# Kernel optimization log

Measured on AMD Instinct MI355X. Metric: run time of the kernel, lower is better.

## Reference

```python
import jax, jax.numpy as jnp
import numpy as np

B, C, H, W = 4, 256, 48, 48
NH = 8
HD = C // NH
SCALE = HD ** -0.5


def setup_inputs() -> dict:
    key = jax.random.key(0)
    ks = jax.random.split(key, 9)
    std = 1.0 / np.sqrt(C)
    return {
        "x": jax.random.normal(ks[0], (B, C, H, W), dtype=jnp.float32),
        "Wq": jax.random.normal(ks[1], (C, C), dtype=jnp.float32) * std,
        "bq": jax.random.normal(ks[2], (C,), dtype=jnp.float32) * std,
        "Wk": jax.random.normal(ks[3], (C, C), dtype=jnp.float32) * std,
        "bk": jax.random.normal(ks[4], (C,), dtype=jnp.float32) * std,
        "Wv": jax.random.normal(ks[5], (C, C), dtype=jnp.float32) * std,
        "bv": jax.random.normal(ks[6], (C,), dtype=jnp.float32) * std,
        "Wo": jax.random.normal(ks[7], (C, C), dtype=jnp.float32) * std,
        "bo": jax.random.normal(ks[8], (C,), dtype=jnp.float32) * std,
    }


def _proj(x, Wm, bm):
    # 1x1 conv == pointwise channel matmul; x: [B,C,H,W], Wm: [out,in]
    return jnp.einsum('bchw,oc->bohw', x, Wm) + bm[None, :, None, None]


def reference(x, Wq, bq, Wk, bk, Wv, bv, Wo, bo):
    b, c, h, w = x.shape
    s = h * w
    # [B,C,H,W] -> [B, NH, S, HD]
    def heads(t):
        return t.reshape(b, NH, HD, s).transpose(0, 1, 3, 2)
    q = heads(_proj(x, Wq, bq))
    k = heads(_proj(x, Wk, bk))
    v = heads(_proj(x, Wv, bv))
    attn = jax.nn.softmax(jnp.einsum('bhsd,bhtd->bhst', q, k) * SCALE, axis=-1)
    out = jnp.einsum('bhst,bhtd->bhsd', attn, v)
    out = out.transpose(0, 1, 3, 2).reshape(b, c, h, w)
    out = _proj(out, Wo, bo)
    return out + x
```

## Files before the change

### kernel.cpp

```cpp
#include <hip/hip_runtime.h>
#include <hip/hip_bf16.h>

#define BATCH 4
#define CCH   256
#define SS    2304
#define NHEAD 8
#define HD    32
#define SCALE_L2E (1.4426950408889634f * 0.17677669529663687f)

using bf16x8 = __attribute__((ext_vector_type(8))) short;
using v4s    = __attribute__((ext_vector_type(4))) short;
using v8s    = __attribute__((ext_vector_type(8))) short;
using f32x4  = __attribute__((ext_vector_type(4))) float;

static __device__ __forceinline__ unsigned short f2bf(float f) {
    union { float f; unsigned u; } a; a.f = f;
    unsigned r = a.u + 0x7fff + ((a.u >> 16) & 1);
    return (unsigned short)(r >> 16);
}
static __device__ __forceinline__ unsigned pk2(float a, float b) {
    return (unsigned)f2bf(a) | ((unsigned)f2bf(b) << 16);
}
static __device__ __forceinline__ v4s pack4(float a, float b, float c, float d) {
    float2 lo; lo.x = a; lo.y = b;
    float2 hi; hi.x = c; hi.y = d;
    union { __hip_bfloat162 h2[2]; v4s s; } u;
    u.h2[0] = __float22bfloat162_rn(lo);
    u.h2[1] = __float22bfloat162_rn(hi);
    return u.s;
}

__global__ __launch_bounds__(256) void wconv(const float* __restrict__ Wq, const float* __restrict__ Wk,
                                             const float* __restrict__ Wv, const float* __restrict__ Wo,
                                             unsigned short* __restrict__ wqkv, unsigned short* __restrict__ wo) {
    const int idx = blockIdx.x * 256 + threadIdx.x;
    if (idx < 768 * 256) {
        const int o = idx >> 8, c = idx & 255;
        const float v = (o < 256) ? Wq[idx] : (o < 512) ? Wk[(o - 256) * 256 + c] : Wv[(o - 512) * 256 + c];
        wqkv[idx] = f2bf(v);
    } else {
        const int j = idx - 768 * 256;
        wo[j] = f2bf(Wo[j]);
    }
}

__global__ __launch_bounds__(256) void xtrans(const float* __restrict__ x, unsigned short* __restrict__ xt) {
    __shared__ float T[64][65];
    const int b = blockIdx.z, c0 = blockIdx.y * 64, s0 = blockIdx.x * 64;
    const int tid = threadIdx.x;
    #pragma unroll
    for (int p = 0; p < 16; ++p) {
        const int c = p * 4 + (tid >> 6), s = tid & 63;
        T[c][s] = x[((size_t)(b * CCH + c0 + c)) * SS + s0 + s];
    }
    __syncthreads();
    #pragma unroll
    for (int p = 0; p < 8; ++p) {
        const int s = p * 8 + (tid >> 5), c = (tid & 31) * 2;
        *(unsigned*)&xt[((size_t)(b * SS + s0 + s)) * CCH + c0 + c] = pk2(T[c][s], T[c + 1][s]);
    }
}

__global__ __launch_bounds__(256) void gemm_qkv(const unsigned short* __restrict__ xt,
                                                const unsigned short* __restrict__ wqkv,
                                                const float* __restrict__ bq, const float* __restrict__ bk,
                                                const float* __restrict__ bv,
                                                unsigned short* __restrict__ qt, unsigned short* __restrict__ kt,
                                                unsigned short* __restrict__ vp) {
    __shared__ char Eb[4][9216];
    const int b  = blockIdx.z;
    const int o0 = blockIdx.x * 64, s0 = blockIdx.y * 128;
    const int tid = threadIdx.x, wid = tid >> 6, lane = tid & 63;
    const int lr = lane & 15, lg = lane >> 4;
    const int o_w = o0 + (wid & 1) * 32, s_w = s0 + (wid >> 1) * 64;

    const f32x4 zero4 = {0.f, 0.f, 0.f, 0.f};
    f32x4 acc[2][4];
    #pragma unroll
    for (int ai = 0; ai < 2; ++ai)
        #pragma unroll
        for (int bj = 0; bj < 4; ++bj) acc[ai][bj] = zero4;

    #pragma unroll
    for (int c0 = 0; c0 < 256; c0 += 32) {
        bf16x8 a[2], bb[4];
        #pragma unroll
        for (int ai = 0; ai < 2; ++ai)
            a[ai] = *(const bf16x8*)&wqkv[(size_t)(o_w + ai * 16 + lr) * 256 + c0 + lg * 8];
        #pragma unroll
        for (int bj = 0; bj < 4; ++bj)
            bb[bj] = *(const bf16x8*)&xt[((size_t)b * SS + s_w + bj * 16 + lr) * 256 + c0 + lg * 8];
        #pragma unroll
        for (int ai = 0; ai < 2; ++ai)
            #pragma unroll
            for (int bj = 0; bj < 4; ++bj)
                acc[ai][bj] = __builtin_amdgcn_mfma_f32_16x16x32_bf16(a[ai], bb[bj], acc[ai][bj], 0, 0, 0);
    }

    const int t = o0 >> 8;
    const int o_loc = o_w - t * 256;
    const float* bias = (t == 0) ? bq : (t == 1) ? bk : bv;

    float vals[2][4][4];
    #pragma unroll
    for (int ai = 0; ai < 2; ++ai)
        #pragma unroll
        for (int bj = 0; bj < 4; ++bj)
            #pragma unroll
            for (int i = 0; i < 4; ++i) {
                float vv = acc[ai][bj][i] + bias[o_loc + ai * 16 + 4 * lg + i];
                if (t == 0) vv *= SCALE_L2E;
                vals[ai][bj][i] = vv;
            }

    if (t < 2) {
        unsigned short* dst = (t == 0) ? qt : kt;
        unsigned short* Ls = (unsigned short*)Eb[wid];
        #pragma unroll
        for (int ai = 0; ai < 2; ++ai)
            #pragma unroll
            for (int bj = 0; bj < 4; ++bj) {
                uint2 w;
                w.x = pk2(vals[ai][bj][0], vals[ai][bj][1]);
                w.y = pk2(vals[ai][bj][2], vals[ai][bj][3]);
                *(uint2*)&Ls[(bj * 16 + lr) * 40 + ai * 16 + 4 * lg] = w;
            }
        const int h = o_loc >> 5;
        const size_t base = (size_t)(b * NHEAD + h) * SS;
        #pragma unroll
        for (int p = 0; p < 4; ++p) {
            const int cid = p * 64 + lane;
            const int s_loc = cid >> 2, oc = cid & 3;
            uint4 v = *(const uint4*)&Ls[s_loc * 40 + oc * 8];
            *(uint4*)&dst[(base + s_w + s_loc) * HD + oc * 8] = v;
        }
    } else {
        float* Lf = (float*)Eb[wid];
        #pragma unroll
        for (int ai = 0; ai < 2; ++ai)
            #pragma unroll
            for (int bj = 0; bj < 4; ++bj)
                #pragma unroll
                for (int i = 0; i < 4; ++i)
                    Lf[(ai * 16 + 4 * lg + i) * 68 + bj * 16 + lr] = vals[ai][bj][i];
        #pragma unroll
        for (int p = 0; p < 4; ++p) {
            const int cid = p * 64 + lane;
            const int oc = cid >> 3, sc8 = (cid & 7) * 8;
            float4 f0 = *(const float4*)&Lf[oc * 68 + sc8];
            float4 f1 = *(const float4*)&Lf[oc * 68 + sc8 + 4];
            uint4 w;
            w.x = pk2(f0.x, f0.y); w.y = pk2(f0.z, f0.w);
            w.z = pk2(f1.x, f1.y); w.w = pk2(f1.z, f1.w);
            *(uint4*)&vp[((size_t)(b * CCH) + o_loc + oc) * SS + s_w + sc8] = w;
        }
    }
}


#define SBAR __builtin_amdgcn_sched_barrier(0)

#define STAGE_LOAD(T0) do {                                                                \
    kreg = *(const v8s*)(ksrc + (size_t)(T0) * HD);                                        \
    vl   = *(const v4s*)(vsrc0 + (T0));                                                    \
    vh   = *(const v4s*)(vsrc1 + (T0));                                                    \
} while (0)

#define STAGE_WRITE(BUF) do {                                                              \
    *(v8s*)&Kbuf[BUF][wid * 512 + lane * 8] = kreg;                                        \
    *(v8s*)&Vbuf[BUF][wid * 512 + lane * 8] =                                              \
        __builtin_shufflevector(vl, vh, 0, 1, 2, 3, 4, 5, 6, 7);                           \
} while (0)

#define ATT_COMPUTE(BUF) do {                                                              \
    bf16x8 KF[4]; v8s VV[4];                                                               \
    _Pragma("unroll") for (int tt = 0; tt < 4; ++tt)                                       \
        KF[tt] = *(const bf16x8*)&Kbuf[BUF][tt * 512 + lane * 8];                          \
    _Pragma("unroll") for (int tt = 0; tt < 4; ++tt)                                       \
        VV[tt] = *(const v8s*)&Vbuf[BUF][tt * 512 + lane * 8];                             \
    f32x4 sc[4];                                                                           \
    _Pragma("unroll") for (int tt = 0; tt < 4; ++tt)                                       \
        sc[tt] = __builtin_amdgcn_mfma_f32_16x16x32_bf16(KF[tt], qf, zero4, 0, 0, 0);      \
    float p[16];                                                                           \
    _Pragma("unroll") for (int tt = 0; tt < 4; ++tt)                                       \
        _Pragma("unroll") for (int i = 0; i < 4; ++i)                                      \
            p[tt * 4 + i] = __builtin_amdgcn_exp2f(sc[tt][i]);                             \
    _Pragma("unroll") for (int tt = 0; tt < 4; ++tt)                                       \
        psum += (p[tt * 4] + p[tt * 4 + 1]) + (p[tt * 4 + 2] + p[tt * 4 + 3]);             \
    _Pragma("unroll") for (int tt = 0; tt < 4; ++tt) {                                     \
        const v4s pf = pack4(p[tt * 4], p[tt * 4 + 1], p[tt * 4 + 2], p[tt * 4 + 3]);      \
        const v4s v0 = __builtin_shufflevector(VV[tt], VV[tt], 0, 1, 2, 3);                \
        const v4s v1 = __builtin_shufflevector(VV[tt], VV[tt], 4, 5, 6, 7);                \
        acc[0] = __builtin_amdgcn_mfma_f32_16x16x16bf16_1k(v0, pf, acc[0], 0, 0, 0);       \
        acc[1] = __builtin_amdgcn_mfma_f32_16x16x16bf16_1k(v1, pf, acc[1], 0, 0, 0);       \
    }                                                                                      \
} while (0)

__global__ __launch_bounds__(256, 4) void attn(const unsigned short* __restrict__ qt,
                                               const unsigned short* __restrict__ kt,
                                               const unsigned short* __restrict__ vp,
                                               unsigned short* __restrict__ ot) {
    __shared__ short Kbuf[2][2048];
    __shared__ short Vbuf[2][2048];

    const int tid = threadIdx.x;
    const int wid = tid >> 6, lane = tid & 63;
    const int lr = lane & 15, lg = lane >> 4;

    const int bid = blockIdx.x;
    const int xs = bid & 7, w = bid >> 3;
    const int bh = xs * 4 + w / 36;
    const int q0 = (w % 36) * 64 + wid * 16;
    const int b  = bh >> 3, h = bh & 7;

    const unsigned short* qtb = qt + (size_t)bh * SS * HD;
    const unsigned short* ktb = kt + (size_t)bh * SS * HD;
    const unsigned short* vb  = vp + (size_t)(b * CCH + h * HD) * SS;

    const unsigned short* ksrc  = ktb + (size_t)(wid * 16 + lr) * HD + lg * 8;
    const unsigned short* vsrc0 = vb + (size_t)lr * SS + wid * 16 + lg * 4;
    const unsigned short* vsrc1 = vb + (size_t)(16 + lr) * SS + wid * 16 + lg * 4;

    const f32x4 zero4 = {0.f, 0.f, 0.f, 0.f};

    bf16x8 qf = *(const bf16x8*)&qtb[(size_t)(q0 + lr) * HD + lg * 8];

    f32x4 acc[2];
    acc[0] = zero4; acc[1] = zero4;
    float psum = 0.f;

    v8s kreg; v4s vl, vh;

    STAGE_LOAD(0);
    STAGE_WRITE(0);
    __syncthreads();

    #pragma unroll 1
    for (int ii = 0; ii < 18; ++ii) {
        STAGE_LOAD((2 * ii + 1) * 64);
        SBAR;
        ATT_COMPUTE(0);
        SBAR;
        STAGE_WRITE(1);
        __syncthreads();
        if (ii < 17) {
            STAGE_LOAD((2 * ii + 2) * 64);
        }
        SBAR;
        ATT_COMPUTE(1);
        SBAR;
        if (ii < 17) {
            STAGE_WRITE(0);
        }
        __syncthreads();
    }

    psum += __shfl_xor(psum, 16);
    psum += __shfl_xor(psum, 32);

    const float inv = 1.f / psum;
    #pragma unroll
    for (int dh = 0; dh < 2; ++dh) {
        const float o0v = acc[dh][0] * inv;
        const float o1v = acc[dh][1] * inv;
        const float o2v = acc[dh][2] * inv;
        const float o3v = acc[dh][3] * inv;
        const v4s sv = pack4(o0v, o1v, o2v, o3v);
        *(v4s*)&ot[((size_t)b * SS + q0 + lr) * CCH + h * HD + dh * 16 + 4 * lg] = sv;
    }
}

__global__ __launch_bounds__(256) void gemm_o(const unsigned short* __restrict__ ot,
                                              const unsigned short* __restrict__ wo,
                                              const float* __restrict__ bo, const float* __restrict__ x,
                                              float* __restrict__ out) {
    const int b  = blockIdx.z;
    const int o0 = blockIdx.x * 64, s0 = blockIdx.y * 128;
    const int tid = threadIdx.x, wid = tid >> 6, lane = tid & 63;
    const int lr = lane & 15, lg = lane >> 4;
    const int o_w = o0 + (wid & 1) * 32, s_w = s0 + (wid >> 1) * 64;

    const f32x4 zero4 = {0.f, 0.f, 0.f, 0.f};
    f32x4 acc[2][4];
    #pragma unroll
    for (int ai = 0; ai < 2; ++ai)
        #pragma unroll
        for (int bj = 0; bj < 4; ++bj) acc[ai][bj] = zero4;

    #pragma unroll
    for (int c0 = 0; c0 < 256; c0 += 32) {
        bf16x8 a[2], bb[4];
        #pragma unroll
        for (int ai = 0; ai < 2; ++ai)
            a[ai] = *(const bf16x8*)&wo[(size_t)(o_w + ai * 16 + lr) * 256 + c0 + lg * 8];
        #pragma unroll
        for (int bj = 0; bj < 4; ++bj)
            bb[bj] = *(const bf16x8*)&ot[((size_t)b * SS + s_w + bj * 16 + lr) * 256 + c0 + lg * 8];
        #pragma unroll
        for (int ai = 0; ai < 2; ++ai)
            #pragma unroll
            for (int bj = 0; bj < 4; ++bj)
                acc[ai][bj] = __builtin_amdgcn_mfma_f32_16x16x32_bf16(a[ai], bb[bj], acc[ai][bj], 0, 0, 0);
    }

    #pragma unroll
    for (int ai = 0; ai < 2; ++ai)
        #pragma unroll
        for (int bj = 0; bj < 4; ++bj)
            #pragma unroll
            for (int i = 0; i < 4; ++i) {
                const int o = o_w + ai * 16 + 4 * lg + i;
                const int s = s_w + bj * 16 + lr;
                const size_t idx = (size_t)(b * CCH + o) * SS + s;
                out[idx] = acc[ai][bj][i] + bo[o] + x[idx];
            }
}

extern "C" void kernel_launch(void* const* d_in, const int* in_sizes, int n_in,
                              void* d_out, int out_size, void* d_ws, size_t ws_size,
                              hipStream_t stream) {
    const float* x  = (const float*)d_in[0];
    const float* Wq = (const float*)d_in[1];
    const float* bq = (const float*)d_in[2];
    const float* Wk = (const float*)d_in[3];
    const float* bk = (const float*)d_in[4];
    const float* Wv = (const float*)d_in[5];
    const float* bv = (const float*)d_in[6];
    const float* Wo = (const float*)d_in[7];
    const float* bo = (const float*)d_in[8];
    float* out = (float*)d_out;

    const size_t plane = (size_t)BATCH * CCH * SS;
    unsigned short* xt   = (unsigned short*)d_ws;
    unsigned short* qtw  = xt  + plane;
    unsigned short* ktw  = qtw + plane;
    unsigned short* vpw  = ktw + plane;
    unsigned short* otw  = vpw + plane;
    unsigned short* wqkv = otw + plane;
    unsigned short* wob  = wqkv + 768 * 256;

    wconv<<<dim3(1024), dim3(256), 0, stream>>>(Wq, Wk, Wv, Wo, wqkv, wob);
    xtrans<<<dim3(SS / 64, CCH / 64, BATCH), dim3(256), 0, stream>>>(x, xt);
    gemm_qkv<<<dim3(12, 18, BATCH), dim3(256), 0, stream>>>(xt, wqkv, bq, bk, bv, qtw, ktw, vpw);
    attn<<<dim3(1152), dim3(256), 0, stream>>>(qtw, ktw, vpw, otw);
    gemm_o<<<dim3(4, 18, BATCH), dim3(256), 0, stream>>>(otw, wob, bo, x, out);
}
```

Measured before the change: 105.4 us.

## Merge weight-convert and x-transpose kernels; deepen attention K/V prefetch with setprio

The weight bf16 conversion and the x transpose now run as one launch, which removes a kernel launch and the gap between the two. The attention loop switches to two register staging sets, so the global load for tile n+2 is issued before tile n is computed. This gives global loads a full compute phase of latency hiding. It also raises wave priority around the MFMA sections and adds register pressure with launch_bounds(256,4), so occupancy could suffer.

Result: no change. 103.5 us (-1.8%).

```diff
diff --git a/kernel.cpp b/kernel.cpp
--- a/kernel.cpp
+++ b/kernel.cpp
@@ -30,34 +30,38 @@
     return u.s;
 }
 
-__global__ __launch_bounds__(256) void wconv(const float* __restrict__ Wq, const float* __restrict__ Wk,
-                                             const float* __restrict__ Wv, const float* __restrict__ Wo,
-                                             unsigned short* __restrict__ wqkv, unsigned short* __restrict__ wo) {
-    const int idx = blockIdx.x * 256 + threadIdx.x;
-    if (idx < 768 * 256) {
-        const int o = idx >> 8, c = idx & 255;
-        const float v = (o < 256) ? Wq[idx] : (o < 512) ? Wk[(o - 256) * 256 + c] : Wv[(o - 512) * 256 + c];
-        wqkv[idx] = f2bf(v);
+__global__ __launch_bounds__(256) void prep(const float* __restrict__ Wq, const float* __restrict__ Wk,
+                                            const float* __restrict__ Wv, const float* __restrict__ Wo,
+                                            const float* __restrict__ x,
+                                            unsigned short* __restrict__ wqkv, unsigned short* __restrict__ wo,
+                                            unsigned short* __restrict__ xt) {
+    __shared__ float T[64][65];
+    const int tid = threadIdx.x;
+    if (blockIdx.x < 1024) {
+        const int idx = blockIdx.x * 256 + tid;
+        if (idx < 768 * 256) {
+            const int o = idx >> 8, c = idx & 255;
+            const float v = (o < 256) ? Wq[idx] : (o < 512) ? Wk[(o - 256) * 256 + c] : Wv[(o - 512) * 256 + c];
+            wqkv[idx] = f2bf(v);
+        } else {
+            const int j = idx - 768 * 256;
+            wo[j] = f2bf(Wo[j]);
+        }
     } else {
-        const int j = idx - 768 * 256;
-        wo[j] = f2bf(Wo[j]);
-    }
-}
-
-__global__ __launch_bounds__(256) void xtrans(const float* __restrict__ x, unsigned short* __restrict__ xt) {
-    __shared__ float T[64][65];
-    const int b = blockIdx.z, c0 = blockIdx.y * 64, s0 = blockIdx.x * 64;
-    const int tid = threadIdx.x;
-    #pragma unroll
-    for (int p = 0; p < 16; ++p) {
-        const int c = p * 4 + (tid >> 6), s = tid & 63;
-        T[c][s] = x[((size_t)(b * CCH + c0 + c)) * SS + s0 + s];
-    }
-    __syncthreads();
-    #pragma unroll
-    for (int p = 0; p < 8; ++p) {
-        const int s = p * 8 + (tid >> 5), c = (tid & 31) * 2;
-        *(unsigned*)&xt[((size_t)(b * SS + s0 + s)) * CCH + c0 + c] = pk2(T[c][s], T[c + 1][s]);
+        const int e = blockIdx.x - 1024;
+        const int b = e / 144, rem = e % 144;
+        const int c0 = (rem / 36) * 64, s0 = (rem % 36) * 64;
+        #pragma unroll
+        for (int p = 0; p < 16; ++p) {
+            const int c = p * 4 + (tid >> 6), s = tid & 63;
+            T[c][s] = x[((size_t)(b * CCH + c0 + c)) * SS + s0 + s];
+        }
+        __syncthreads();
+        #pragma unroll
+        for (int p = 0; p < 8; ++p) {
+            const int s = p * 8 + (tid >> 5), c = (tid & 31) * 2;
+            *(unsigned*)&xt[((size_t)(b * SS + s0 + s)) * CCH + c0 + c] = pk2(T[c][s], T[c + 1][s]);
+        }
     }
 }
 
@@ -160,16 +164,28 @@
 
 #define SBAR __builtin_amdgcn_sched_barrier(0)
 
-#define STAGE_LOAD(T0) do {                                                                \
-    kreg = *(const v8s*)(ksrc + (size_t)(T0) * HD);                                        \
-    vl   = *(const v4s*)(vsrc0 + (T0));                                                    \
-    vh   = *(const v4s*)(vsrc1 + (T0));                                                    \
-} while (0)
-
-#define STAGE_WRITE(BUF) do {                                                              \
-    *(v8s*)&Kbuf[BUF][wid * 512 + lane * 8] = kreg;                                        \
+#define STAGE_LOAD_A(T0) do {                                                              \
+    kregA = *(const v8s*)(ksrc + (size_t)(T0) * HD);                                       \
+    vlA   = *(const v4s*)(vsrc0 + (T0));                                                   \
+    vhA   = *(const v4s*)(vsrc1 + (T0));                                                   \
+} while (0)
+
+#define STAGE_LOAD_B(T0) do {                                                              \
+    kregB = *(const v8s*)(ksrc + (size_t)(T0) * HD);                                       \
+    vlB   = *(const v4s*)(vsrc0 + (T0));                                                   \
+    vhB   = *(const v4s*)(vsrc1 + (T0));                                                   \
+} while (0)
+
+#define STAGE_WRITE_A(BUF) do {                                                            \
+    *(v8s*)&Kbuf[BUF][wid * 512 + lane * 8] = kregA;                                       \
     *(v8s*)&Vbuf[BUF][wid * 512 + lane * 8] =                                              \
-        __builtin_shufflevector(vl, vh, 0, 1, 2, 3, 4, 5, 6, 7);                           \
+        __builtin_shufflevector(vlA, vhA, 0, 1, 2, 3, 4, 5, 6, 7);                         \
+} while (0)
+
+#define STAGE_WRITE_B(BUF) do {                                                            \
+    *(v8s*)&Kbuf[BUF][wid * 512 + lane * 8] = kregB;                                       \
+    *(v8s*)&Vbuf[BUF][wid * 512 + lane * 8] =                                              \
+        __builtin_shufflevector(vlB, vhB, 0, 1, 2, 3, 4, 5, 6, 7);                         \
 } while (0)
 
 #define ATT_COMPUTE(BUF) do {                                                              \
@@ -178,6 +194,7 @@
         KF[tt] = *(const bf16x8*)&Kbuf[BUF][tt * 512 + lane * 8];                          \
     _Pragma("unroll") for (int tt = 0; tt < 4; ++tt)                                       \
         VV[tt] = *(const v8s*)&Vbuf[BUF][tt * 512 + lane * 8];                             \
+    __builtin_amdgcn_s_setprio(1);                                                         \
     f32x4 sc[4];                                                                           \
     _Pragma("unroll") for (int tt = 0; tt < 4; ++tt)                                       \
         sc[tt] = __builtin_amdgcn_mfma_f32_16x16x32_bf16(KF[tt], qf, zero4, 0, 0, 0);      \
@@ -194,6 +211,7 @@
         acc[0] = __builtin_amdgcn_mfma_f32_16x16x16bf16_1k(v0, pf, acc[0], 0, 0, 0);       \
         acc[1] = __builtin_amdgcn_mfma_f32_16x16x16bf16_1k(v1, pf, acc[1], 0, 0, 0);       \
     }                                                                                      \
+    __builtin_amdgcn_s_setprio(0);                                                         \
 } while (0)
 
 __global__ __launch_bounds__(256, 4) void attn(const unsigned short* __restrict__ qt,
@@ -229,31 +247,31 @@
     acc[0] = zero4; acc[1] = zero4;
     float psum = 0.f;
 
-    v8s kreg; v4s vl, vh;
-
-    STAGE_LOAD(0);
-    STAGE_WRITE(0);
+    v8s kregA, kregB; v4s vlA, vhA, vlB, vhB;
+
+    STAGE_LOAD_A(0);
+    STAGE_WRITE_A(0);
+    STAGE_LOAD_B(64);
     __syncthreads();
 
     #pragma unroll 1
-    for (int ii = 0; ii < 18; ++ii) {
-        STAGE_LOAD((2 * ii + 1) * 64);
+    for (int ii = 0; ii < 17; ++ii) {
+        STAGE_WRITE_B(1);
+        STAGE_LOAD_A((2 * ii + 2) * 64);
         SBAR;
         ATT_COMPUTE(0);
-        SBAR;
-        STAGE_WRITE(1);
         __syncthreads();
-        if (ii < 17) {
-            STAGE_LOAD((2 * ii + 2) * 64);
-        }
+        STAGE_WRITE_A(0);
+        STAGE_LOAD_B((2 * ii + 3) * 64);
         SBAR;
         ATT_COMPUTE(1);
-        SBAR;
-        if (ii < 17) {
-            STAGE_WRITE(0);
-        }
         __syncthreads();
     }
+    STAGE_WRITE_B(1);
+    SBAR;
+    ATT_COMPUTE(0);
+    __syncthreads();
+    ATT_COMPUTE(1);
 
     psum += __shfl_xor(psum, 16);
     psum += __shfl_xor(psum, 32);
@@ -339,8 +357,7 @@
     unsigned short* wqkv = otw + plane;
     unsigned short* wob  = wqkv + 768 * 256;
 
-    wconv<<<dim3(1024), dim3(256), 0, stream>>>(Wq, Wk, Wv, Wo, wqkv, wob);
-    xtrans<<<dim3(SS / 64, CCH / 64, BATCH), dim3(256), 0, stream>>>(x, xt);
+    prep<<<dim3(1600), dim3(256), 0, stream>>>(Wq, Wk, Wv, Wo, x, wqkv, wob, xt);
     gemm_qkv<<<dim3(12, 18, BATCH), dim3(256), 0, stream>>>(xt, wqkv, bq, bk, bv, qtw, ktw, vpw);
     attn<<<dim3(1152), dim3(256), 0, stream>>>(qtw, ktw, vpw, otw);
     gemm_o<<<dim3(4, 18, BATCH), dim3(256), 0, stream>>>(otw, wob, bo, x, out);
```
